# Optimization experiments

Measured on AMD Instinct MI355X. Metric: run time of the kernel, lower is better.

Reference implementation:

```python
import jax, jax.numpy as jnp
import numpy as np

NV = 117000
NE = 468000
EMB = 300
IN_DIM = 768
BATCH = 4096
HID = 500
NUM_LABELS = 2


def setup_inputs() -> dict:
    key = jax.random.key(0)
    ks = jax.random.split(key, 12)
    inp = {
        "input_tensor": jax.random.normal(ks[0], (BATCH, IN_DIM), dtype=jnp.float32),
        "node": jax.random.randint(ks[1], (BATCH,), 0, NV, dtype=jnp.int64),
        "edge_row": jax.random.randint(ks[2], (NE,), 0, NV, dtype=jnp.int32),
        "edge_col": jax.random.randint(ks[3], (NE,), 0, NV, dtype=jnp.int32),
        # learned parameters
        "H0": jax.random.normal(ks[4], (NV, EMB), dtype=jnp.float32) * 1.0,
        "W1": jax.random.normal(ks[5], (EMB, EMB), dtype=jnp.float32) * 0.01,
        "W2": jax.random.normal(ks[6], (EMB, EMB), dtype=jnp.float32) * 0.01,
        "Wa": jax.random.normal(ks[7], (IN_DIM + EMB, HID), dtype=jnp.float32) * 0.03,
        "ba": jnp.zeros((HID,), dtype=jnp.float32),
        "Wb": jax.random.normal(ks[8], (HID, HID), dtype=jnp.float32) * 0.04,
        "bb": jnp.zeros((HID,), dtype=jnp.float32),
        "Wc": jax.random.normal(ks[9], (HID, NUM_LABELS), dtype=jnp.float32) * 0.04,
        "bc": jnp.zeros((NUM_LABELS,), dtype=jnp.float32),
    }
    return inp


def reference(input_tensor, node, edge_row, edge_col, H0, W1, W2, Wa, ba, Wb, bb, Wc, bc):
    nV = H0.shape[0]
    # symmetric normalization D^{-1/2} A D^{-1/2} from edge list (duplicates sum, as in csr)
    deg = jax.ops.segment_sum(jnp.ones_like(edge_row, dtype=H0.dtype), edge_row, num_segments=nV)
    dinv = jnp.where(deg > 0, deg ** -0.5, 0.0)
    vals = dinv[edge_row] * dinv[edge_col]  # [nE]

    def spmm(X):  # LM @ X via gather + segment_sum
        return jax.ops.segment_sum(vals[:, None] * X[edge_col], edge_row, num_segments=nV)

    H1 = jax.nn.sigmoid(spmm(H0 @ W1))        # [nV, EMB]
    H2 = jax.nn.sigmoid(spmm(H1 @ W2))        # [nV, EMB]
    fc = jnp.concatenate([H2[node], input_tensor], axis=1)  # [B, EMB+IN_DIM]
    h = jax.nn.sigmoid(fc @ Wa + ba)
    h = jax.nn.sigmoid(h @ Wb + bb)
    return h @ Wc + bc                        # [B, NUM_LABELS]
```

## Files before the change

kernel.cpp:

```cpp
#include <hip/hip_runtime.h>
#include <hip/hip_bf16.h>

typedef __hip_bfloat16 bf16;

#define NVX 117000
#define NEX 468000
#define EMB 300
#define STR 320
#define IN_DIM 768
#define BATCH 4096
#define HID 500
#define FCK 1088
#define HPAD 512
#define NB 458

#define CAP1 32768
#define CAP2 4096

#define PRE_W12 (384*STR)
#define PRE_WA  (HPAD*FCK)
#define PRE_WB  (HPAD*HPAD)
#define PRE_TOT (2*PRE_W12 + PRE_WA + PRE_WB)

typedef __attribute__((ext_vector_type(8))) short frag8;
typedef __attribute__((ext_vector_type(4))) float f32x4;

__device__ __forceinline__ float sigmoidf_(float x){ return 1.0f/(1.0f + __expf(-x)); }
__device__ __forceinline__ float bfs2f(short s){
  return __uint_as_float(((unsigned int)(unsigned short)s) << 16);
}
__device__ __forceinline__ short f2bfs(float f){
  bf16 b = __float2bfloat16(f);
  return *(short*)&b;
}

__device__ __forceinline__ void gload_lds16(const bf16* g, bf16* l){
  __builtin_amdgcn_global_load_lds((const __attribute__((address_space(1))) void*)g,
                                   (__attribute__((address_space(3))) void*)l, 16, 0, 0);
}


__global__ void k_deg(const int* __restrict__ erow, int* __restrict__ deg){
  int i = blockIdx.x*blockDim.x + threadIdx.x;
  if (i < NEX) atomicAdd(&deg[erow[i]], 1);
}

__global__ __launch_bounds__(256) void k_partsum(const int* __restrict__ deg,
                                                 float* __restrict__ dinv,
                                                 int* __restrict__ bsum){
  __shared__ int s[256];
  int t = threadIdx.x;
  int i = blockIdx.x*256 + t;
  int d = (i < NVX) ? deg[i] : 0;
  if (i < NVX) dinv[i] = d > 0 ? rsqrtf((float)d) : 0.0f;
  s[t] = d;
  __syncthreads();
  #pragma unroll
  for (int off=128; off; off>>=1){
    if (t < off) s[t] += s[t+off];
    __syncthreads();
  }
  if (t == 0) bsum[blockIdx.x] = s[0];
}

__global__ __launch_bounds__(512) void k_scanb(const int* __restrict__ bsum,
                                               int* __restrict__ boff){
  __shared__ int s[512];
  int t = threadIdx.x;
  int v = (t < NB) ? bsum[t] : 0;
  s[t] = v; __syncthreads();
  #pragma unroll
  for (int off=1; off<512; off<<=1){
    int u = (t>=off) ? s[t-off] : 0;
    __syncthreads();
    s[t] += u;
    __syncthreads();
  }
  if (t < NB) boff[t] = s[t] - v;
}

__global__ __launch_bounds__(256) void k_writeptr(const int* __restrict__ deg,
                                                  const int* __restrict__ boff,
                                                  int* __restrict__ rowptr,
                                                  int* __restrict__ cursor){
  __shared__ int s[256];
  int t = threadIdx.x;
  int i = blockIdx.x*256 + t;
  int v = (i < NVX) ? deg[i] : 0;
  s[t] = v; __syncthreads();
  #pragma unroll
  for (int off=1; off<256; off<<=1){
    int u = (t>=off) ? s[t-off] : 0;
    __syncthreads();
    s[t] += u;
    __syncthreads();
  }
  if (i < NVX){
    int e = boff[blockIdx.x] + s[t] - v;
    rowptr[i] = e;
    cursor[i] = e;
  }
}

__global__ void k_scatter(const int* __restrict__ erow, const int* __restrict__ ecol,
                          const float* __restrict__ dinv, int* __restrict__ cursor,
                          int* __restrict__ ccol, float* __restrict__ cval){
  int i = blockIdx.x*blockDim.x + threadIdx.x;
  if (i < NEX){
    int r = erow[i], c = ecol[i];
    int p = atomicAdd(&cursor[r], 1);
    ccol[p] = c;
    cval[p] = dinv[r]*dinv[c];
  }
}


__global__ void k_flag2(const int* __restrict__ node, int* __restrict__ flag2){
  int i = blockIdx.x*blockDim.x + threadIdx.x;
  if (i < BATCH) flag2[node[i]] = 1;
}

__global__ void k_flag1(const int* __restrict__ erow, const int* __restrict__ ecol,
                        const int* __restrict__ flag2, int* __restrict__ flag1){
  int i = blockIdx.x*blockDim.x + threadIdx.x;
  if (i < NEX && flag2[erow[i]]) flag1[ecol[i]] = 1;
}

__global__ void k_compact(const int* __restrict__ flag1, const int* __restrict__ flag2,
                          int* __restrict__ L1, int* __restrict__ inv1,
                          int* __restrict__ L2, int* __restrict__ inv2,
                          int* __restrict__ counts){
  int v = blockIdx.x*blockDim.x + threadIdx.x;
  if (v >= NVX) return;
  if (flag1[v]){ int idx = atomicAdd(&counts[0], 1); L1[idx] = v; inv1[v] = idx; }
  if (flag2[v]){ int idx = atomicAdd(&counts[1], 1); L2[idx] = v; inv2[v] = idx; }
}


__global__ __launch_bounds__(256) void k_prep(const float* __restrict__ W1,
                                              const float* __restrict__ W2,
                                              const float* __restrict__ Wa,
                                              const float* __restrict__ Wb,
                                              bf16* __restrict__ Wt1,
                                              bf16* __restrict__ Wt2,
                                              bf16* __restrict__ Wat,
                                              bf16* __restrict__ Wbt){
  long i = (long)blockIdx.x*256 + threadIdx.x;
  if (i < 2*PRE_W12){
    const float* W = (i < PRE_W12) ? W1 : W2;
    bf16* o = (i < PRE_W12) ? Wt1 : Wt2;
    int j = (int)((i < PRE_W12) ? i : i - PRE_W12);
    int n = j / STR, k = j % STR;
    float v = (n < EMB && k < EMB) ? W[k*EMB + n] : 0.0f;
    o[j] = __float2bfloat16(v);
    return;
  }
  i -= 2*PRE_W12;
  if (i < PRE_WA){
    int n = (int)(i / FCK), k = (int)(i % FCK);
    float v = 0.0f;
    if (n < HID){
      if (k < EMB)        v = Wa[(size_t)k*HID + n];
      else if (k >= STR)  v = Wa[(size_t)(k-(STR-EMB))*HID + n];
    }
    Wat[i] = __float2bfloat16(v);
    return;
  }
  i -= PRE_WA;
  if (i < PRE_WB){
    int n = (int)(i / HPAD), k = (int)(i % HPAD);
    float v = (n < HID && k < HID) ? Wb[(size_t)k*HID + n] : 0.0f;
    Wbt[i] = __float2bfloat16(v);
  }
}


__global__ __launch_bounds__(256) void k_spmm1(const int* __restrict__ rowptr,
                                               const int* __restrict__ ccol,
                                               const float* __restrict__ cval,
                                               const float* __restrict__ H0,
                                               const int* __restrict__ L1,
                                               const int* __restrict__ counts,
                                               bf16* __restrict__ Gc1){
  int i = (int)((blockIdx.x*blockDim.x + threadIdx.x) >> 6);
  int lane = threadIdx.x & 63;
  if (lane >= 40) return;
  int n1 = counts[0];
  int n1pad = (n1 + 127) & ~127;
  if (i >= n1pad) return;
  int c0 = lane*8;
  bool hv1 = (c0 + 3) < EMB;
  bool hv2 = (c0 + 7) < EMB;
  float acc[8] = {0.f,0.f,0.f,0.f,0.f,0.f,0.f,0.f};
  if (i < n1 && hv1){
    int v = L1[i];
    int e0 = rowptr[v], e1 = rowptr[v+1];
    int e = e0;
    for (; e + 1 < e1; e += 2){
      float va = cval[e], vb = cval[e+1];
      const float* xa = H0 + (size_t)ccol[e  ]*EMB + c0;
      const float* xb = H0 + (size_t)ccol[e+1]*EMB + c0;
      float4 a0 = *(const float4*)xa;
      float4 b0 = *(const float4*)xb;
      float4 a1 = hv2 ? *(const float4*)(xa+4) : make_float4(0,0,0,0);
      float4 b1 = hv2 ? *(const float4*)(xb+4) : make_float4(0,0,0,0);
      acc[0] += va*a0.x + vb*b0.x;  acc[1] += va*a0.y + vb*b0.y;
      acc[2] += va*a0.z + vb*b0.z;  acc[3] += va*a0.w + vb*b0.w;
      acc[4] += va*a1.x + vb*b1.x;  acc[5] += va*a1.y + vb*b1.y;
      acc[6] += va*a1.z + vb*b1.z;  acc[7] += va*a1.w + vb*b1.w;
    }
    if (e < e1){
      float va = cval[e];
      const float* xa = H0 + (size_t)ccol[e]*EMB + c0;
      float4 a0 = *(const float4*)xa;
      float4 a1 = hv2 ? *(const float4*)(xa+4) : make_float4(0,0,0,0);
      acc[0] += va*a0.x; acc[1] += va*a0.y; acc[2] += va*a0.z; acc[3] += va*a0.w;
      acc[4] += va*a1.x; acc[5] += va*a1.y; acc[6] += va*a1.z; acc[7] += va*a1.w;
    }
  }
  frag8 o;
  #pragma unroll
  for (int j=0;j<8;++j) o[j] = f2bfs(acc[j]);
  *(frag8*)(Gc1 + (size_t)i*STR + c0) = o;
}


__global__ __launch_bounds__(256) void k_spmm2(const int* __restrict__ rowptr,
                                               const int* __restrict__ ccol,
                                               const float* __restrict__ cval,
                                               const bf16* __restrict__ Hc1,
                                               const int* __restrict__ inv1,
                                               const int* __restrict__ L2,
                                               const int* __restrict__ counts,
                                               bf16* __restrict__ Gc2){
  int i = (int)((blockIdx.x*blockDim.x + threadIdx.x) >> 6);
  int lane = threadIdx.x & 63;
  if (lane >= 40) return;
  int n2 = counts[1];
  int n2pad = (n2 + 127) & ~127;
  if (i >= n2pad) return;
  float acc[8] = {0.f,0.f,0.f,0.f,0.f,0.f,0.f,0.f};
  if (i < n2){
    int v = L2[i];
    int e0 = rowptr[v], e1 = rowptr[v+1];
    int e = e0;
    for (; e + 1 < e1; e += 2){
      float va = cval[e], vb = cval[e+1];
      frag8 xa = *(const frag8*)(Hc1 + (size_t)inv1[ccol[e  ]]*STR + lane*8);
      frag8 xb = *(const frag8*)(Hc1 + (size_t)inv1[ccol[e+1]]*STR + lane*8);
      #pragma unroll
      for (int j=0;j<8;++j) acc[j] += va*bfs2f(xa[j]) + vb*bfs2f(xb[j]);
    }
    if (e < e1){
      float va = cval[e];
      frag8 xa = *(const frag8*)(Hc1 + (size_t)inv1[ccol[e]]*STR + lane*8);
      #pragma unroll
      for (int j=0;j<8;++j) acc[j] += va*bfs2f(xa[j]);
    }
  }
  frag8 o;
  #pragma unroll
  for (int j=0;j<8;++j) o[j] = f2bfs(acc[j]);
  *(frag8*)(Gc2 + (size_t)i*STR + lane*8) = o;
}


__global__ __launch_bounds__(256) void k_gemm_node(const bf16* __restrict__ A,
                                                   const bf16* __restrict__ Wt,
                                                   bf16* __restrict__ C,
                                                   const int* __restrict__ counts, int which){
  const int row0 = blockIdx.y * 128;
  if (row0 >= counts[which]) return;
  __shared__ bf16 As[128*32];
  __shared__ bf16 Bs[128*32];
  const int tid  = threadIdx.x;
  const int wv   = tid >> 6;
  const int lane = tid & 63;
  const int n0   = blockIdx.x * 128;
  const int wm = wv & 1, wn = wv >> 1;
  const int srow = lane >> 2;
  const int schk = lane & 3;
  const int fr = lane & 15, fq = lane >> 4;

  f32x4 acc[4][4];
  #pragma unroll
  for (int i=0;i<4;++i)
    #pragma unroll
    for (int j=0;j<4;++j) acc[i][j] = (f32x4)(0.0f);

  for (int k0 = 0; k0 < STR; k0 += 32){
    const bf16* ag = A + (size_t)(row0 + wv*16 + srow)*STR + k0 + schk*8;
    gload_lds16(ag,           As + wv*512 + lane*8);
    gload_lds16(ag + 64*STR,  As + 2048 + wv*512 + lane*8);
    const bf16* bg = Wt + (size_t)(n0 + wv*16 + srow)*STR + k0 + schk*8;
    gload_lds16(bg,           Bs + wv*512 + lane*8);
    gload_lds16(bg + 64*STR,  Bs + 2048 + wv*512 + lane*8);
    __syncthreads();
    frag8 a[4], b[4];
    #pragma unroll
    for (int mi=0;mi<4;++mi)
      a[mi] = *(const frag8*)(As + (wm*64 + mi*16 + fr)*32 + fq*8);
    #pragma unroll
    for (int ni=0;ni<4;++ni)
      b[ni] = *(const frag8*)(Bs + (wn*64 + ni*16 + fr)*32 + fq*8);
    #pragma unroll
    for (int mi=0;mi<4;++mi)
      #pragma unroll
      for (int ni=0;ni<4;++ni)
        acc[mi][ni] = __builtin_amdgcn_mfma_f32_16x16x32_bf16(a[mi], b[ni], acc[mi][ni], 0, 0, 0);
    __syncthreads();
  }

  #pragma unroll
  for (int mi=0;mi<4;++mi){
    int row = row0 + wm*64 + mi*16 + fq*4;
    #pragma unroll
    for (int ni=0;ni<4;++ni){
      int col = n0 + wn*64 + ni*16 + fr;
      if (col < STR){
        bf16* cp = C + (size_t)row*STR + col;
        #pragma unroll
        for (int r=0;r<4;++r){
          float v = (col < EMB) ? sigmoidf_(acc[mi][ni][r]) : 0.0f;
          cp[(size_t)r*STR] = __float2bfloat16(v);
        }
      }
    }
  }
}


__global__ __launch_bounds__(256) void k_fc1g(const bf16* __restrict__ Hc2,
                                              const int* __restrict__ node,
                                              const int* __restrict__ inv2,
                                              const float* __restrict__ input,
                                              const bf16* __restrict__ Wat,
                                              const float* __restrict__ ba,
                                              bf16* __restrict__ h1){
  __shared__ bf16 As[128*32];
  __shared__ bf16 Bs[128*32];
  const int tid  = threadIdx.x;
  const int wv   = tid >> 6;
  const int lane = tid & 63;
  const int row0 = blockIdx.y * 128;
  const int n0   = blockIdx.x * 128;
  const int wm = wv & 1, wn = wv >> 1;
  const int srow = lane >> 2;
  const int schk = lane & 3;
  const int fr = lane & 15, fq = lane >> 4;

  const int nlo = inv2[node[row0 + wv*16 + srow]];
  const int nhi = inv2[node[row0 + 64 + wv*16 + srow]];

  f32x4 acc[4][4];
  #pragma unroll
  for (int i=0;i<4;++i)
    #pragma unroll
    for (int j=0;j<4;++j) acc[i][j] = (f32x4)(0.0f);

  for (int k0 = 0; k0 < FCK; k0 += 32){
    if (k0 < STR){
      gload_lds16(Hc2 + (size_t)nlo*STR + k0 + schk*8, As + wv*512 + lane*8);
      gload_lds16(Hc2 + (size_t)nhi*STR + k0 + schk*8, As + 2048 + wv*512 + lane*8);
    } else {
      int c = k0 - STR + schk*8;
      int m0 = wv*16 + srow;
      float4 u0 = *(const float4*)(input + (size_t)(row0+m0)*IN_DIM + c);
      float4 u1 = *(const float4*)(input + (size_t)(row0+m0)*IN_DIM + c + 4);
      frag8 t0;
      t0[0]=f2bfs(u0.x); t0[1]=f2bfs(u0.y); t0[2]=f2bfs(u0.z); t0[3]=f2bfs(u0.w);
      t0[4]=f2bfs(u1.x); t0[5]=f2bfs(u1.y); t0[6]=f2bfs(u1.z); t0[7]=f2bfs(u1.w);
      *(frag8*)(As + m0*32 + schk*8) = t0;
      int m1 = 64 + wv*16 + srow;
      float4 u2 = *(const float4*)(input + (size_t)(row0+m1)*IN_DIM + c);
      float4 u3 = *(const float4*)(input + (size_t)(row0+m1)*IN_DIM + c + 4);
      frag8 t1;
      t1[0]=f2bfs(u2.x); t1[1]=f2bfs(u2.y); t1[2]=f2bfs(u2.z); t1[3]=f2bfs(u2.w);
      t1[4]=f2bfs(u3.x); t1[5]=f2bfs(u3.y); t1[6]=f2bfs(u3.z); t1[7]=f2bfs(u3.w);
      *(frag8*)(As + m1*32 + schk*8) = t1;
    }
    gload_lds16(Wat + (size_t)(n0 + wv*16 + srow)*FCK + k0 + schk*8, Bs + wv*512 + lane*8);
    gload_lds16(Wat + (size_t)(n0 + 64 + wv*16 + srow)*FCK + k0 + schk*8, Bs + 2048 + wv*512 + lane*8);
    __syncthreads();
    frag8 a[4], b[4];
    #pragma unroll
    for (int mi=0;mi<4;++mi)
      a[mi] = *(const frag8*)(As + (wm*64 + mi*16 + fr)*32 + fq*8);
    #pragma unroll
    for (int ni=0;ni<4;++ni)
      b[ni] = *(const frag8*)(Bs + (wn*64 + ni*16 + fr)*32 + fq*8);
    #pragma unroll
    for (int mi=0;mi<4;++mi)
      #pragma unroll
      for (int ni=0;ni<4;++ni)
        acc[mi][ni] = __builtin_amdgcn_mfma_f32_16x16x32_bf16(a[mi], b[ni], acc[mi][ni], 0, 0, 0);
    __syncthreads();
  }

  #pragma unroll
  for (int mi=0;mi<4;++mi){
    int row = row0 + wm*64 + mi*16 + fq*4;
    #pragma unroll
    for (int ni=0;ni<4;++ni){
      int col = n0 + wn*64 + ni*16 + fr;
      float bv = (col < HID) ? ba[col] : 0.0f;
      bf16* cp = h1 + (size_t)row*HPAD + col;
      #pragma unroll
      for (int r=0;r<4;++r)
        cp[(size_t)r*HPAD] = __float2bfloat16(sigmoidf_(acc[mi][ni][r] + bv));
    }
  }
}


__global__ __launch_bounds__(256) void k_fc2o(const bf16* __restrict__ A,
                                              const bf16* __restrict__ B,
                                              const float* __restrict__ bb,
                                              const float* __restrict__ Wc,
                                              const float* __restrict__ bc,
                                              float* __restrict__ out){
  __shared__ bf16 As[128*32];
  __shared__ bf16 Bs[128*32];
  const int tid  = threadIdx.x;
  const int wv   = tid >> 6;
  const int lane = tid & 63;
  const int row0 = blockIdx.y * 128;
  const int n0   = blockIdx.x * 128;
  const int wm = wv & 1, wn = wv >> 1;
  const int srow = lane >> 2;
  const int schk = lane & 3;
  const int fr = lane & 15, fq = lane >> 4;

  f32x4 acc[4][4];
  #pragma unroll
  for (int i=0;i<4;++i)
    #pragma unroll
    for (int j=0;j<4;++j) acc[i][j] = (f32x4)(0.0f);

  for (int k0 = 0; k0 < HPAD; k0 += 32){
    const bf16* ag = A + (size_t)(row0 + wv*16 + srow)*HPAD + k0 + schk*8;
    gload_lds16(ag,            As + wv*512 + lane*8);
    gload_lds16(ag + 64*HPAD,  As + 2048 + wv*512 + lane*8);
    const bf16* bg = B + (size_t)(n0 + wv*16 + srow)*HPAD + k0 + schk*8;
    gload_lds16(bg,            Bs + wv*512 + lane*8);
    gload_lds16(bg + 64*HPAD,  Bs + 2048 + wv*512 + lane*8);
    __syncthreads();
    frag8 a[4], b[4];
    #pragma unroll
    for (int mi=0;mi<4;++mi)
      a[mi] = *(const frag8*)(As + (wm*64 + mi*16 + fr)*32 + fq*8);
    #pragma unroll
    for (int ni=0;ni<4;++ni)
      b[ni] = *(const frag8*)(Bs + (wn*64 + ni*16 + fr)*32 + fq*8);
    #pragma unroll
    for (int mi=0;mi<4;++mi)
      #pragma unroll
      for (int ni=0;ni<4;++ni)
        acc[mi][ni] = __builtin_amdgcn_mfma_f32_16x16x32_bf16(a[mi], b[ni], acc[mi][ni], 0, 0, 0);
    __syncthreads();
  }

  #pragma unroll
  for (int mi=0;mi<4;++mi){
    #pragma unroll
    for (int r=0;r<4;++r){
      int row = row0 + wm*64 + mi*16 + fq*4 + r;
      float s0 = 0.0f, s1 = 0.0f;
      #pragma unroll
      for (int ni=0;ni<4;++ni){
        int col = n0 + wn*64 + ni*16 + fr;
        if (col < HID){
          float v = sigmoidf_(acc[mi][ni][r] + bb[col]);
          s0 += v * Wc[col*2+0];
          s1 += v * Wc[col*2+1];
        }
      }
      #pragma unroll
      for (int off=1; off<16; off<<=1){
        s0 += __shfl_xor(s0, off);
        s1 += __shfl_xor(s1, off);
      }
      if (fr == 0){
        if (n0 == 0 && wn == 0){ s0 += bc[0]; s1 += bc[1]; }
        atomicAdd(out + (size_t)row*2 + 0, s0);
        atomicAdd(out + (size_t)row*2 + 1, s1);
      }
    }
  }
}


extern "C" void kernel_launch(void* const* d_in, const int* in_sizes, int n_in,
                              void* d_out, int out_size, void* d_ws, size_t ws_size,
                              hipStream_t stream){
  const float* input = (const float*)d_in[0];
  const int*   node  = (const int*)d_in[1];
  const int*   erow  = (const int*)d_in[2];
  const int*   ecol  = (const int*)d_in[3];
  const float* H0    = (const float*)d_in[4];
  const float* W1    = (const float*)d_in[5];
  const float* W2    = (const float*)d_in[6];
  const float* Wa    = (const float*)d_in[7];
  const float* ba    = (const float*)d_in[8];
  const float* Wb    = (const float*)d_in[9];
  const float* bb    = (const float*)d_in[10];
  const float* Wc    = (const float*)d_in[11];
  const float* bc    = (const float*)d_in[12];

  char* p = (char*)d_ws;
  auto alloc = [&](size_t bytes)->char*{ char* r = p; p += (bytes + 255) & ~(size_t)255; return r; };
  char* z0     = p;
  int*   deg    = (int*)  alloc((size_t)NVX*4);
  int*   flag1  = (int*)  alloc((size_t)NVX*4);
  int*   flag2  = (int*)  alloc((size_t)NVX*4);
  int*   counts = (int*)  alloc(256);
  size_t zlen   = (size_t)(p - z0);
  float* dinv   = (float*)alloc((size_t)NVX*4);
  int*   rowptr = (int*)  alloc((size_t)(NVX+1)*4);
  int*   cursor = (int*)  alloc((size_t)NVX*4);
  int*   bsum   = (int*)  alloc((size_t)NB*4);
  int*   boff   = (int*)  alloc((size_t)NB*4);
  int*   ccol   = (int*)  alloc((size_t)NEX*4);
  float* cval   = (float*)alloc((size_t)NEX*4);
  int*   L1     = (int*)  alloc((size_t)CAP1*4);
  int*   inv1   = (int*)  alloc((size_t)NVX*4);
  int*   L2     = (int*)  alloc((size_t)CAP2*4);
  int*   inv2   = (int*)  alloc((size_t)NVX*4);
  bf16*  Gc1    = (bf16*) alloc((size_t)CAP1*STR*2);
  bf16*  Hc1    = (bf16*) alloc((size_t)CAP1*STR*2);
  bf16*  Gc2    = (bf16*) alloc((size_t)CAP2*STR*2);
  bf16*  Hc2    = (bf16*) alloc((size_t)CAP2*STR*2);
  bf16*  Wt1    = (bf16*) alloc((size_t)384*STR*2);
  bf16*  Wt2    = (bf16*) alloc((size_t)384*STR*2);
  bf16*  Wat    = (bf16*) alloc((size_t)HPAD*FCK*2);
  bf16*  Wbt    = (bf16*) alloc((size_t)HPAD*HPAD*2);
  bf16*  h1     = (bf16*) alloc((size_t)BATCH*HPAD*2);

  hipMemsetAsync(z0, 0, zlen, stream);
  hipMemsetAsync(d_out, 0, (size_t)out_size*4, stream);

  k_deg     <<<(NEX+255)/256, 256, 0, stream>>>(erow, deg);
  k_partsum <<<NB, 256, 0, stream>>>(deg, dinv, bsum);
  k_scanb   <<<1, 512, 0, stream>>>(bsum, boff);
  k_writeptr<<<NB, 256, 0, stream>>>(deg, boff, rowptr, cursor);
  k_scatter <<<(NEX+255)/256, 256, 0, stream>>>(erow, ecol, dinv, cursor, ccol, cval);

  k_flag2  <<<(BATCH+255)/256, 256, 0, stream>>>(node, flag2);
  k_flag1  <<<(NEX+255)/256, 256, 0, stream>>>(erow, ecol, flag2, flag1);
  k_compact<<<(NVX+255)/256, 256, 0, stream>>>(flag1, flag2, L1, inv1, L2, inv2, counts);

  k_prep<<<(PRE_TOT+255)/256, 256, 0, stream>>>(W1, W2, Wa, Wb, Wt1, Wt2, Wat, Wbt);

  k_spmm1    <<<CAP1/4, 256, 0, stream>>>(rowptr, ccol, cval, H0, L1, counts, Gc1);
  k_gemm_node<<<dim3(3, CAP1/128), 256, 0, stream>>>(Gc1, Wt1, Hc1, counts, 0);
  k_spmm2    <<<CAP2/4, 256, 0, stream>>>(rowptr, ccol, cval, Hc1, inv1, L2, counts, Gc2);
  k_gemm_node<<<dim3(3, CAP2/128), 256, 0, stream>>>(Gc2, Wt2, Hc2, counts, 1);

  k_fc1g<<<dim3(HPAD/128, BATCH/128), 256, 0, stream>>>(Hc2, node, inv2, input, Wat, ba, h1);
  k_fc2o<<<dim3(HPAD/128, BATCH/128), 256, 0, stream>>>(h1, Wbt, bb, Wc, bc, (float*)d_out);
}
```

Measured before the change: 439.3 us.

## Fuse graph preprocessing kernels and scatter only edges of needed rows

Merges the nine preprocessing launches (degree count, partial sums, scan, row pointers, scatter, flags, compaction, weight prep) into four fused kernels. The block-offset scan is folded into the row-pointer kernel, with each block summing the preceding block totals itself. The CSR scatter now writes only edges whose row is flagged as needed by the two sparse layers, which cuts atomics and writes. The change also adds capacity clamps on the compacted lists, and it leaves the CSR for unused rows incomplete.

```diff
diff --git a/kernel.cpp b/kernel.cpp
--- a/kernel.cpp
+++ b/kernel.cpp
@@ -13,6 +13,7 @@
 #define FCK 1088
 #define HPAD 512
 #define NB 458
+#define NEB 1829
 
 #define CAP1 32768
 #define CAP2 4096
@@ -21,6 +22,7 @@
 #define PRE_WA  (HPAD*FCK)
 #define PRE_WB  (HPAD*HPAD)
 #define PRE_TOT (2*PRE_W12 + PRE_WA + PRE_WB)
+#define PRE_BLK ((PRE_TOT+255)/256)
 
 typedef __attribute__((ext_vector_type(8))) short frag8;
 typedef __attribute__((ext_vector_type(4))) float f32x4;
@@ -40,112 +42,22 @@
 }
 
 
-__global__ void k_deg(const int* __restrict__ erow, int* __restrict__ deg){
-  int i = blockIdx.x*blockDim.x + threadIdx.x;
+__global__ __launch_bounds__(256) void k_setup(const int* __restrict__ erow,
+                                               const int* __restrict__ node,
+                                               int* __restrict__ deg,
+                                               int* __restrict__ flag2,
+                                               const float* __restrict__ W1,
+                                               const float* __restrict__ W2,
+                                               const float* __restrict__ Wa,
+                                               const float* __restrict__ Wb,
+                                               bf16* __restrict__ Wt1,
+                                               bf16* __restrict__ Wt2,
+                                               bf16* __restrict__ Wat,
+                                               bf16* __restrict__ Wbt){
+  long i = (long)blockIdx.x*256 + threadIdx.x;
   if (i < NEX) atomicAdd(&deg[erow[i]], 1);
-}
-
-__global__ __launch_bounds__(256) void k_partsum(const int* __restrict__ deg,
-                                                 float* __restrict__ dinv,
-                                                 int* __restrict__ bsum){
-  __shared__ int s[256];
-  int t = threadIdx.x;
-  int i = blockIdx.x*256 + t;
-  int d = (i < NVX) ? deg[i] : 0;
-  if (i < NVX) dinv[i] = d > 0 ? rsqrtf((float)d) : 0.0f;
-  s[t] = d;
-  __syncthreads();
-  #pragma unroll
-  for (int off=128; off; off>>=1){
-    if (t < off) s[t] += s[t+off];
-    __syncthreads();
-  }
-  if (t == 0) bsum[blockIdx.x] = s[0];
-}
-
-__global__ __launch_bounds__(512) void k_scanb(const int* __restrict__ bsum,
-                                               int* __restrict__ boff){
-  __shared__ int s[512];
-  int t = threadIdx.x;
-  int v = (t < NB) ? bsum[t] : 0;
-  s[t] = v; __syncthreads();
-  #pragma unroll
-  for (int off=1; off<512; off<<=1){
-    int u = (t>=off) ? s[t-off] : 0;
-    __syncthreads();
-    s[t] += u;
-    __syncthreads();
-  }
-  if (t < NB) boff[t] = s[t] - v;
-}
-
-__global__ __launch_bounds__(256) void k_writeptr(const int* __restrict__ deg,
-                                                  const int* __restrict__ boff,
-                                                  int* __restrict__ rowptr,
-                                                  int* __restrict__ cursor){
-  __shared__ int s[256];
-  int t = threadIdx.x;
-  int i = blockIdx.x*256 + t;
-  int v = (i < NVX) ? deg[i] : 0;
-  s[t] = v; __syncthreads();
-  #pragma unroll
-  for (int off=1; off<256; off<<=1){
-    int u = (t>=off) ? s[t-off] : 0;
-    __syncthreads();
-    s[t] += u;
-    __syncthreads();
-  }
-  if (i < NVX){
-    int e = boff[blockIdx.x] + s[t] - v;
-    rowptr[i] = e;
-    cursor[i] = e;
-  }
-}
-
-__global__ void k_scatter(const int* __restrict__ erow, const int* __restrict__ ecol,
-                          const float* __restrict__ dinv, int* __restrict__ cursor,
-                          int* __restrict__ ccol, float* __restrict__ cval){
-  int i = blockIdx.x*blockDim.x + threadIdx.x;
-  if (i < NEX){
-    int r = erow[i], c = ecol[i];
-    int p = atomicAdd(&cursor[r], 1);
-    ccol[p] = c;
-    cval[p] = dinv[r]*dinv[c];
-  }
-}
-
-
-__global__ void k_flag2(const int* __restrict__ node, int* __restrict__ flag2){
-  int i = blockIdx.x*blockDim.x + threadIdx.x;
   if (i < BATCH) flag2[node[i]] = 1;
-}
-
-__global__ void k_flag1(const int* __restrict__ erow, const int* __restrict__ ecol,
-                        const int* __restrict__ flag2, int* __restrict__ flag1){
-  int i = blockIdx.x*blockDim.x + threadIdx.x;
-  if (i < NEX && flag2[erow[i]]) flag1[ecol[i]] = 1;
-}
-
-__global__ void k_compact(const int* __restrict__ flag1, const int* __restrict__ flag2,
-                          int* __restrict__ L1, int* __restrict__ inv1,
-                          int* __restrict__ L2, int* __restrict__ inv2,
-                          int* __restrict__ counts){
-  int v = blockIdx.x*blockDim.x + threadIdx.x;
-  if (v >= NVX) return;
-  if (flag1[v]){ int idx = atomicAdd(&counts[0], 1); L1[idx] = v; inv1[v] = idx; }
-  if (flag2[v]){ int idx = atomicAdd(&counts[1], 1); L2[idx] = v; inv2[v] = idx; }
-}
-
-
-__global__ __launch_bounds__(256) void k_prep(const float* __restrict__ W1,
-                                              const float* __restrict__ W2,
-                                              const float* __restrict__ Wa,
-                                              const float* __restrict__ Wb,
-                                              bf16* __restrict__ Wt1,
-                                              bf16* __restrict__ Wt2,
-                                              bf16* __restrict__ Wat,
-                                              bf16* __restrict__ Wbt){
-  long i = (long)blockIdx.x*256 + threadIdx.x;
+
   if (i < 2*PRE_W12){
     const float* W = (i < PRE_W12) ? W1 : W2;
     bf16* o = (i < PRE_W12) ? Wt1 : Wt2;
@@ -171,6 +83,101 @@
     int n = (int)(i / HPAD), k = (int)(i % HPAD);
     float v = (n < HID && k < HID) ? Wb[(size_t)k*HID + n] : 0.0f;
     Wbt[i] = __float2bfloat16(v);
+  }
+}
+
+
+__global__ __launch_bounds__(256) void k_flag1ps(const int* __restrict__ erow,
+                                                 const int* __restrict__ ecol,
+                                                 const int* __restrict__ flag2,
+                                                 const int* __restrict__ deg,
+                                                 int* __restrict__ flag1,
+                                                 float* __restrict__ dinv,
+                                                 int* __restrict__ bsum){
+  int t = threadIdx.x;
+  long j = (long)blockIdx.x*256 + t;
+  if (j < NEX && flag2[erow[j]]) flag1[ecol[j]] = 1;
+
+  if (blockIdx.x < NB){
+    __shared__ int s[256];
+    int i = blockIdx.x*256 + t;
+    int d = (i < NVX) ? deg[i] : 0;
+    if (i < NVX) dinv[i] = d > 0 ? rsqrtf((float)d) : 0.0f;
+    s[t] = d;
+    __syncthreads();
+    #pragma unroll
+    for (int off=128; off; off>>=1){
+      if (t < off) s[t] += s[t+off];
+      __syncthreads();
+    }
+    if (t == 0) bsum[blockIdx.x] = s[0];
+  }
+}
+
+
+__global__ __launch_bounds__(256) void k_writeptr2(const int* __restrict__ deg,
+                                                   const int* __restrict__ bsum,
+                                                   int* __restrict__ rowptr,
+                                                   int* __restrict__ cursor){
+  __shared__ int sb[256];
+  __shared__ int s[256];
+  int t = threadIdx.x;
+  int b = blockIdx.x;
+  int acc = 0;
+  for (int j = t; j < b; j += 256) acc += bsum[j];
+  sb[t] = acc;
+  __syncthreads();
+  #pragma unroll
+  for (int off=128; off; off>>=1){
+    if (t < off) sb[t] += sb[t+off];
+    __syncthreads();
+  }
+  int boff = sb[0];
+
+  int i = b*256 + t;
+  int v = (i < NVX) ? deg[i] : 0;
+  s[t] = v; __syncthreads();
+  #pragma unroll
+  for (int off=1; off<256; off<<=1){
+    int u = (t>=off) ? s[t-off] : 0;
+    __syncthreads();
+    s[t] += u;
+    __syncthreads();
+  }
+  if (i < NVX){
+    int e = boff + s[t] - v;
+    rowptr[i] = e;
+    cursor[i] = e;
+  }
+  if (b == 0 && t == 0) rowptr[NVX] = NEX;
+}
+
+
+__global__ __launch_bounds__(256) void k_edgec(const int* __restrict__ erow,
+                                               const int* __restrict__ ecol,
+                                               const float* __restrict__ dinv,
+                                               const int* __restrict__ flag1,
+                                               const int* __restrict__ flag2,
+                                               int* __restrict__ cursor,
+                                               int* __restrict__ ccol,
+                                               float* __restrict__ cval,
+                                               int* __restrict__ L1, int* __restrict__ inv1,
+                                               int* __restrict__ L2, int* __restrict__ inv2,
+                                               int* __restrict__ counts){
+  long j = (long)blockIdx.x*256 + threadIdx.x;
+  if (j < NEX){
+    int r = erow[j];
+    if (flag1[r] | flag2[r]){
+      int c = ecol[j];
+      int p = atomicAdd(&cursor[r], 1);
+      ccol[p] = c;
+      cval[p] = dinv[r]*dinv[c];
+    }
+  }
+  int v = (int)j;
+  if (v < NVX){
+    if (flag1[v]){ int idx = atomicAdd(&counts[0], 1); if (idx < CAP1){ L1[idx] = v; inv1[v] = idx; } }
+    if (flag2[v]){ int idx = atomicAdd(&counts[1], 1); if (idx < CAP2){ L2[idx] = v; inv2[v] = idx; } }
   }
 }
 
@@ -185,7 +192,7 @@
   int i = (int)((blockIdx.x*blockDim.x + threadIdx.x) >> 6);
   int lane = threadIdx.x & 63;
   if (lane >= 40) return;
-  int n1 = counts[0];
+  int n1 = counts[0]; if (n1 > CAP1) n1 = CAP1;
   int n1pad = (n1 + 127) & ~127;
   if (i >= n1pad) return;
   int c0 = lane*8;
@@ -236,7 +243,7 @@
   int i = (int)((blockIdx.x*blockDim.x + threadIdx.x) >> 6);
   int lane = threadIdx.x & 63;
   if (lane >= 40) return;
-  int n2 = counts[1];
+  int n2 = counts[1]; if (n2 > CAP2) n2 = CAP2;
   int n2pad = (n2 + 127) & ~127;
   if (i >= n2pad) return;
   float acc[8] = {0.f,0.f,0.f,0.f,0.f,0.f,0.f,0.f};
@@ -519,7 +526,6 @@
   int*   rowptr = (int*)  alloc((size_t)(NVX+1)*4);
   int*   cursor = (int*)  alloc((size_t)NVX*4);
   int*   bsum   = (int*)  alloc((size_t)NB*4);
-  int*   boff   = (int*)  alloc((size_t)NB*4);
   int*   ccol   = (int*)  alloc((size_t)NEX*4);
   float* cval   = (float*)alloc((size_t)NEX*4);
   int*   L1     = (int*)  alloc((size_t)CAP1*4);
@@ -539,17 +545,11 @@
   hipMemsetAsync(z0, 0, zlen, stream);
   hipMemsetAsync(d_out, 0, (size_t)out_size*4, stream);
 
-  k_deg     <<<(NEX+255)/256, 256, 0, stream>>>(erow, deg);
-  k_partsum <<<NB, 256, 0, stream>>>(deg, dinv, bsum);
-  k_scanb   <<<1, 512, 0, stream>>>(bsum, boff);
-  k_writeptr<<<NB, 256, 0, stream>>>(deg, boff, rowptr, cursor);
-  k_scatter <<<(NEX+255)/256, 256, 0, stream>>>(erow, ecol, dinv, cursor, ccol, cval);
-
-  k_flag2  <<<(BATCH+255)/256, 256, 0, stream>>>(node, flag2);
-  k_flag1  <<<(NEX+255)/256, 256, 0, stream>>>(erow, ecol, flag2, flag1);
-  k_compact<<<(NVX+255)/256, 256, 0, stream>>>(flag1, flag2, L1, inv1, L2, inv2, counts);
-
-  k_prep<<<(PRE_TOT+255)/256, 256, 0, stream>>>(W1, W2, Wa, Wb, Wt1, Wt2, Wat, Wbt);
+  k_setup<<<PRE_BLK, 256, 0, stream>>>(erow, node, deg, flag2, W1, W2, Wa, Wb, Wt1, Wt2, Wat, Wbt);
+  k_flag1ps<<<NEB, 256, 0, stream>>>(erow, ecol, flag2, deg, flag1, dinv, bsum);
+  k_writeptr2<<<NB, 256, 0, stream>>>(deg, bsum, rowptr, cursor);
+  k_edgec<<<NEB, 256, 0, stream>>>(erow, ecol, dinv, flag1, flag2, cursor, ccol, cval,
+                                   L1, inv1, L2, inv2, counts);
 
   k_spmm1    <<<CAP1/4, 256, 0, stream>>>(rowptr, ccol, cval, H0, L1, counts, Gc1);
   k_gemm_node<<<dim3(3, CAP1/128), 256, 0, stream>>>(Gc1, Wt1, Hc1, counts, 0);
```

Result: faster. 407.7 us (-7.2%).
